# Optimization experiments

Measured on AMD Instinct MI355X. Metric: run time of the kernel, lower is better.

Reference implementation:

```python
import jax, jax.numpy as jnp
import numpy as np

B, S, D, H = 4, 2048, 2048, 16
Dh = D // H
BASE = 10000.0


def _rope_tables(seq_len, head_dim, dtype=jnp.float32):
    inv_freq = 1.0 / (BASE ** (jnp.arange(0, head_dim, 2, dtype=jnp.float32) / head_dim))
    t = jnp.arange(seq_len, dtype=jnp.float32)
    freqs = jnp.outer(t, inv_freq)              # [S, Dh/2]
    emb = jnp.concatenate([freqs, freqs], -1)   # [S, Dh]
    return jnp.cos(emb).astype(dtype), jnp.sin(emb).astype(dtype)


def _rotate_half(x):
    d = x.shape[-1] // 2
    return jnp.concatenate([-x[..., d:], x[..., :d]], axis=-1)


def setup_inputs() -> dict:
    key = jax.random.key(0)
    ks = jax.random.split(key, 5)
    std = D ** -0.5
    x = jax.random.normal(ks[0], (B, S, D), jnp.float32)
    Wq = jax.random.normal(ks[1], (D, D), jnp.float32) * std
    Wk = jax.random.normal(ks[2], (D, D), jnp.float32) * std
    Wv = jax.random.normal(ks[3], (D, D), jnp.float32) * std
    Wo = jax.random.normal(ks[4], (D, D), jnp.float32) * std
    attn_mask = jnp.triu(jnp.ones((S, S), dtype=bool), k=1)  # True = masked (causal)
    return {"x": x, "attn_mask": attn_mask, "Wq": Wq, "Wk": Wk, "Wv": Wv, "Wo": Wo}


def reference(x, attn_mask, Wq, Wk, Wv, Wo):
    b, s, d = x.shape
    # projections (nn.Linear: x @ W.T), split heads -> [B, H, S, Dh]
    q = (x @ Wq.T).reshape(b, s, H, Dh).transpose(0, 2, 1, 3)
    k = (x @ Wk.T).reshape(b, s, H, Dh).transpose(0, 2, 1, 3)
    v = (x @ Wv.T).reshape(b, s, H, Dh).transpose(0, 2, 1, 3)
    cos, sin = _rope_tables(s, Dh, x.dtype)     # [S, Dh]
    q = q * cos + _rotate_half(q) * sin
    k = k * cos + _rotate_half(k) * sin
    scale = Dh ** -0.5
    scores = jnp.einsum('bhqd,bhkd->bhqk', q, k) * scale
    scores = jnp.where(attn_mask[None, None, :, :], -jnp.inf, scores)
    weights = jax.nn.softmax(scores, axis=-1)
    out = jnp.einsum('bhqk,bhkd->bhqd', weights, v)
    out = out.transpose(0, 2, 1, 3).reshape(b, s, d)
    return out @ Wo.T
```

## Files before the change

kernel.cpp:

```cpp
#include <hip/hip_runtime.h>
#include <cstdint>
#include <cmath>

#define NB 4
#define NS 2048
#define ND 2048
#define NH 16
#define NDH 128
#define NM (NB*NS)

typedef unsigned short u16;
typedef __bf16 bf16x8 __attribute__((ext_vector_type(8)));
typedef u16    u16x8  __attribute__((ext_vector_type(8)));
typedef u16    u16x4  __attribute__((ext_vector_type(4)));
typedef float  f32x4  __attribute__((ext_vector_type(4)));
typedef float  f32x16 __attribute__((ext_vector_type(16)));
typedef unsigned u32x4_t __attribute__((ext_vector_type(4)));

__device__ __forceinline__ u16 f2bf(float f) {
  unsigned u = __float_as_uint(f);
  u += 0x7fffu + ((u >> 16) & 1u);
  return (u16)(u >> 16);
}
__device__ __forceinline__ float bf2f(u16 h) {
  return __uint_as_float(((unsigned)h) << 16);
}
__device__ __forceinline__ void gld16(const void* g, void* l) {
  __builtin_amdgcn_global_load_lds((__attribute__((address_space(1))) void*)g,
                                   (__attribute__((address_space(3))) void*)l,
                                   16, 0, 0);
}
__device__ __forceinline__ f32x4 mfma_bf16(bf16x8 a, bf16x8 b, f32x4 c) {
  return __builtin_amdgcn_mfma_f32_16x16x32_bf16(a, b, c, 0, 0, 0);
}
__device__ __forceinline__ f32x16 mfma32_bf16(bf16x8 a, bf16x8 b, f32x16 c) {
  return __builtin_amdgcn_mfma_f32_32x32x16_bf16(a, b, c, 0, 0, 0);
}
__device__ __forceinline__ unsigned cvtpk(float lo, float hi) {
  unsigned r;
  asm("v_cvt_pk_bf16_f32 %0, %1, %2" : "=v"(r) : "v"(lo), "v"(hi));
  return r;
}
__device__ __forceinline__ void p32swap(unsigned &a, unsigned &b) {
  asm volatile("v_permlane32_swap_b32 %0, %1" : "+v"(a), "+v"(b));
}

__global__ void cvt_bf16_kernel(const float* __restrict__ in, u16* __restrict__ out, int n8) {
  int i = blockIdx.x * 256 + threadIdx.x;
  if (i >= n8) return;
  const float4* p = (const float4*)in + (size_t)i * 2;
  float4 a = p[0], b = p[1];
  u16x8 r;
  r[0]=f2bf(a.x); r[1]=f2bf(a.y); r[2]=f2bf(a.z); r[3]=f2bf(a.w);
  r[4]=f2bf(b.x); r[5]=f2bf(b.y); r[6]=f2bf(b.z); r[7]=f2bf(b.w);
  ((u16x8*)out)[i] = r;
}

__global__ void rope_tables_kernel(float* __restrict__ cosT, float* __restrict__ sinT) {
  int s = blockIdx.x, d = threadIdx.x;
  double inv = pow(10000.0, -(double)d / 64.0);
  float ang = (float)((double)s * inv);
  cosT[s*64 + d] = cosf(ang);
  sinT[s*64 + d] = sinf(ang);
}

__global__ void rope_apply_kernel(u16* __restrict__ X, const float* __restrict__ cosT,
                                  const float* __restrict__ sinT) {
  int idx = blockIdx.x * 256 + threadIdx.x;
  int pc = idx & 7, h = (idx >> 3) & (NH - 1), m = idx >> 7;
  int s = m & (NS - 1);
  int d0 = pc * 8;
  size_t base = (size_t)m * ND + h * NDH + d0;
  u16x8 v0 = *(const u16x8*)(X + base);
  u16x8 v1 = *(const u16x8*)(X + base + 64);
  u16x8 r0, r1;
#pragma unroll
  for (int j = 0; j < 8; ++j) {
    float c  = cosT[s*64 + d0 + j];
    float sn = sinT[s*64 + d0 + j];
    float x0 = bf2f(v0[j]), x1 = bf2f(v1[j]);
    r0[j] = f2bf(x0 * c - x1 * sn);
    r1[j] = f2bf(x1 * c + x0 * sn);
  }
  *(u16x8*)(X + base)      = r0;
  *(u16x8*)(X + base + 64) = r1;
}

#define G_PHASE(BUF, KS, MH, LOADB, WAITV, STAGE) do {                            \
  bf16x8 af[4];                                                                   \
  _Pragma("unroll")                                                               \
  for (int mf = 0; mf < 4; ++mf)                                                  \
    af[mf] = *(const bf16x8*)(Asb + (BUF)*32768 + (KS)*16384 + arow + ((MH)*4+mf)*1024); \
  if (LOADB) {                                                                    \
    _Pragma("unroll")                                                             \
    for (int nf = 0; nf < 4; ++nf)                                                \
      bfr[nf] = *(const bf16x8*)(Bsb + (BUF)*32768 + (KS)*16384 + brow + nf*1024); \
  }                                                                               \
  STAGE;                                                                          \
  __builtin_amdgcn_s_setprio(1);                                                  \
  _Pragma("unroll")                                                               \
  for (int mf = 0; mf < 4; ++mf)                                                  \
    _Pragma("unroll")                                                             \
    for (int nf = 0; nf < 4; ++nf)                                                \
      acc[(MH)*4+mf][nf] = mfma_bf16(af[mf], bfr[nf], acc[(MH)*4+mf][nf]);        \
  __builtin_amdgcn_s_setprio(0);                                                  \
  if (WAITV) {                                                                    \
    asm volatile("s_waitcnt vmcnt(4)" ::: "memory");                              \
    __builtin_amdgcn_sched_barrier(0);                                            \
  }                                                                               \
  __builtin_amdgcn_s_barrier();                                                   \
  __builtin_amdgcn_sched_barrier(0);                                              \
} while (0)

template <typename OutT>
__global__ __launch_bounds__(512, 1) void gemm256_kernel(
    const u16* __restrict__ A, const u16* __restrict__ Bw, OutT* __restrict__ C,
    int Nd, int Kd) {
  __shared__ __align__(16) char Asb[65536];
  __shared__ __align__(16) char Bsb[65536];
  int tid = threadIdx.x;
  int wave = tid >> 6, lane = tid & 63;
  int li = lane & 15, lg = lane >> 4;
  int wr = wave >> 2, wc = wave & 3;
  int NTn = Nd >> 8;
  int cpx = (int)gridDim.x >> 3;
  int bid = (int)blockIdx.x;
  int swz = (bid & 7) * cpx + (bid >> 3);
  int m0 = (swz / NTn) << 8, n0 = (swz % NTn) << 8;

  int rswz = (lg * 16) ^ ((li & 3) << 4);
  int arow = (wr * 128 + li) * 64 + rswz;
  int brow = (wc *  64 + li) * 64 + rswz;

  int srow = wave * 16 + (lane >> 2);
  int scswz = ((lane & 3) * 16) ^ ((srow & 3) << 4);
  size_t rowB = (size_t)Kd * 2;
  const char* Asrc = (const char*)A + (size_t)(m0 + srow) * rowB + scswz;
  const char* Bsrc = (const char*)Bw + (size_t)(n0 + srow) * rowB + scswz;
  char* Adst = Asb + wave * 1024;
  char* Bdst = Bsb + wave * 1024;
  size_t half2 = rowB << 7;

  auto stageA = [&](int buf, int ks, int tile) {
    const char* s = Asrc + (size_t)tile * 128 + ks * 64;
    char* d = Adst + buf * 32768 + ks * 16384;
    gld16(s, d);
    gld16(s + half2, d + 8192);
  };
  auto stageB = [&](int buf, int ks, int tile) {
    const char* s = Bsrc + (size_t)tile * 128 + ks * 64;
    char* d = Bdst + buf * 32768 + ks * 16384;
    gld16(s, d);
    gld16(s + half2, d + 8192);
  };

  f32x4 acc[8][4] = {};
  bf16x8 bfr[4];

  int NKT = Kd >> 6;
  int NIT = NKT >> 1;

  stageA(0, 0, 0); stageA(0, 1, 0); stageB(0, 0, 0); stageB(0, 1, 0);
  stageA(1, 0, 1); stageB(1, 0, 1);
  asm volatile("s_waitcnt vmcnt(4)" ::: "memory");
  __builtin_amdgcn_sched_barrier(0);
  __builtin_amdgcn_s_barrier();
  __builtin_amdgcn_sched_barrier(0);

  for (int j = 0; j < NIT; ++j) {
    int t1  = 2*j + 1;
    int tn0 = (2*j + 2) & (NKT - 1);
    int tn1 = (2*j + 3) & (NKT - 1);
    G_PHASE(0, 0, 0, true,  false, { stageA(1, 1, t1);  });
    G_PHASE(0, 0, 1, false, false, { stageB(1, 1, t1);  });
    G_PHASE(0, 1, 1, true,  false, { stageA(0, 0, tn0); });
    G_PHASE(0, 1, 0, false, true,  { stageB(0, 0, tn0); });
    G_PHASE(1, 0, 0, true,  false, { stageA(0, 1, tn0); });
    G_PHASE(1, 0, 1, false, false, { stageB(0, 1, tn0); });
    G_PHASE(1, 1, 1, true,  false, { stageA(1, 0, tn1); });
    G_PHASE(1, 1, 0, false, true,  { stageB(1, 0, tn1); });
  }
  asm volatile("s_waitcnt vmcnt(0)" ::: "memory");

  int rbase = m0 + wr*128 + lg*4;
  int cbase = n0 + wc*64 + li;
#pragma unroll
  for (int am = 0; am < 8; ++am)
#pragma unroll
    for (int nf = 0; nf < 4; ++nf)
#pragma unroll
      for (int r = 0; r < 4; ++r) {
        size_t off = (size_t)(rbase + am*16 + r) * Nd + (cbase + nf*16);
        if constexpr (sizeof(OutT) == 2) C[off] = f2bf(acc[am][nf][r]);
        else                             C[off] = acc[am][nf][r];
      }
}

__global__ __launch_bounds__(512, 2) void flash_attn_kernel(
    const u16* __restrict__ Q, const u16* __restrict__ K, const u16* __restrict__ V,
    u16* __restrict__ O) {
  __shared__ __align__(16) u16 Ks[2*64*128];
  __shared__ __align__(16) u16 Vt[2*128*64];
  int tid = threadIdx.x, wv = tid >> 6, lane = tid & 63;
  int ql = lane & 31, hi = lane >> 5;
  int b = blockIdx.x >> 4, h = blockIdx.x & 15;
  int qt = (int)gridDim.y - 1 - (int)blockIdx.y;
  int q0 = qt << 8;
  int qw = q0 + wv*32;
  int qa = qw + ql;
  int swzl = (ql & 7) << 4;
  const float qscale = 0.08838834764831845f * 1.4426950408889634f;

  bf16x8 qf[8];
  {
    const u16* qp = Q + (size_t)(b*NS + qa) * ND + h*NDH + hi*8;
#pragma unroll
    for (int ds = 0; ds < 8; ++ds) {
      u16x8 t = *(const u16x8*)(qp + ds*16);
      u16x8 r;
#pragma unroll
      for (int j = 0; j < 8; ++j) r[j] = f2bf(bf2f(t[j]) * qscale);
      qf[ds] = *(bf16x8*)&r;
    }
  }
  f32x16 o0 = {}, o1 = {}, o2 = {}, o3 = {};
  float m_run = -INFINITY, l_run = 0.f;

  const char* Kg = (const char*)(K + (size_t)b*NS*ND + h*NDH);
  const char* Vg = (const char*)(V + (size_t)b*NS*ND + h*NDH);
  const int ROWB = ND * 2;

  int p   = tid & 31;
  int kvg = tid >> 5;

  auto issueKV = [&](int kv0, int buf, unsigned (&dlo)[4], unsigned (&dhi)[4]) {
    const char* vrow = Vg + (size_t)(kv0 + kvg*4) * ROWB;
#pragma unroll
    for (int j = 0; j < 4; ++j) {
      dlo[j] = *(const unsigned*)(vrow + j*ROWB + p*4);
      dhi[j] = *(const unsigned*)(vrow + j*ROWB + 128 + p*4);
    }
    char* ksb = (char*)Ks + buf*16384;
#pragma unroll
    for (int c = 0; c < 2; ++c) {
      int s = c*8192 + wv*1024 + lane*16;
      int row = s >> 8;
      int within = (s & 255) ^ ((row & 7) << 4);
      gld16(Kg + (size_t)(kv0 + row)*ROWB + within, ksb + c*8192 + wv*1024);
    }
    __builtin_amdgcn_sched_barrier(0);
  };

  auto dostep = [&](int kv0, int buf, const unsigned (&dlo)[4], const unsigned (&dhi)[4],
                    bool hasNext) {
    if (hasNext) asm volatile("s_waitcnt vmcnt(10)" ::: "memory");
    else         asm volatile("s_waitcnt vmcnt(0)"  ::: "memory");
    __builtin_amdgcn_sched_barrier(0);
    __builtin_amdgcn_s_barrier();
    __builtin_amdgcn_sched_barrier(0);

    char* vtb = (char*)Vt + buf*16384;
    const char* ksb = (const char*)Ks + buf*16384;

    {
      u16x4 rA, rB, rC, rD;
#pragma unroll
      for (int j = 0; j < 4; ++j) {
        rA[j] = (u16)dlo[j]; rB[j] = (u16)(dlo[j] >> 16);
        rC[j] = (u16)dhi[j]; rD[j] = (u16)(dhi[j] >> 16);
      }
      int a0 = ((2*p   )*128 + kvg*8) ^ (((2*p  ) & 7) << 4);
      int a1 = ((2*p+ 1)*128 + kvg*8) ^ (((2*p+1) & 7) << 4);
      int a2 = ((2*p+64)*128 + kvg*8) ^ (((2*p  ) & 7) << 4);
      int a3 = ((2*p+65)*128 + kvg*8) ^ (((2*p+1) & 7) << 4);
      *(u16x4*)(vtb + a0) = rA;
      *(u16x4*)(vtb + a1) = rB;
      *(u16x4*)(vtb + a2) = rC;
      *(u16x4*)(vtb + a3) = rD;
    }

    f32x16 p0 = {}, p1 = {};
    __builtin_amdgcn_s_setprio(1);
#pragma unroll
    for (int ds = 0; ds < 8; ++ds) {
      bf16x8 kf0 = *(const bf16x8*)(ksb + ((ql*256 + ds*32 + hi*16) ^ swzl));
      p0 = mfma32_bf16(kf0, qf[ds], p0);
      bf16x8 kf1 = *(const bf16x8*)(ksb + (((32+ql)*256 + ds*32 + hi*16) ^ swzl));
      p1 = mfma32_bf16(kf1, qf[ds], p1);
    }
    __builtin_amdgcn_s_setprio(0);

    if (kv0 + 63 > qw) {
      int thresh = qa - kv0 - 4*hi;
#pragma unroll
      for (int r = 0; r < 16; ++r) {
        int c0 = (r & 3) + 8*(r >> 2);
        p0[r] = (c0      > thresh) ? -INFINITY : p0[r];
        p1[r] = (c0 + 32 > thresh) ? -INFINITY : p1[r];
      }
    }

    float mx[16];
#pragma unroll
    for (int r = 0; r < 16; ++r) mx[r] = fmaxf(p0[r], p1[r]);
#pragma unroll
    for (int s = 8; s > 0; s >>= 1)
#pragma unroll
      for (int r = 0; r < 8; ++r) if (r < s) mx[r] = fmaxf(mx[r], mx[r + s]);
    float pmax = fmaxf(mx[0], __shfl_xor(mx[0], 32, 64));

    if (!__all(pmax <= m_run + 8.f)) {
      float mn = fmaxf(m_run, pmax);
      float corr = __builtin_amdgcn_exp2f(m_run - mn);
      m_run = mn; l_run *= corr;
#pragma unroll
      for (int r = 0; r < 16; ++r) {
        float cw = __shfl(corr, (r & 3) + 8*(r >> 2) + 4*hi, 64);
        o0[r] *= cw; o1[r] *= cw; o2[r] *= cw; o3[r] *= cw;
      }
    }

    float sm[16];
#pragma unroll
    for (int r = 0; r < 16; ++r) {
      p0[r] = __builtin_amdgcn_exp2f(p0[r] - m_run);
      p1[r] = __builtin_amdgcn_exp2f(p1[r] - m_run);
      sm[r] = p0[r] + p1[r];
    }
#pragma unroll
    for (int s = 8; s > 0; s >>= 1)
#pragma unroll
      for (int r = 0; r < 8; ++r) if (r < s) sm[r] += sm[r + s];
    l_run += sm[0] + __shfl_xor(sm[0], 32, 64);

    bf16x8 pa0, pa1, pa2, pa3;
#define MKPA(P, B, OUT) {                              \
      unsigned a0 = cvtpk(P[(B)+0], P[(B)+1]);         \
      unsigned b0 = cvtpk(P[(B)+4], P[(B)+5]);         \
      p32swap(a0, b0);                                 \
      unsigned a1 = cvtpk(P[(B)+2], P[(B)+3]);         \
      unsigned b1 = cvtpk(P[(B)+6], P[(B)+7]);         \
      p32swap(a1, b1);                                 \
      u32x4_t w; w[0]=a0; w[1]=a1; w[2]=b0; w[3]=b1;   \
      OUT = *(bf16x8*)&w; }
    MKPA(p0, 0, pa0)
    MKPA(p0, 8, pa1)
    MKPA(p1, 0, pa2)
    MKPA(p1, 8, pa3)
#undef MKPA

    asm volatile("s_waitcnt lgkmcnt(0)" ::: "memory");
    __builtin_amdgcn_sched_barrier(0);
    __builtin_amdgcn_s_barrier();
    __builtin_amdgcn_sched_barrier(0);

    __builtin_amdgcn_s_setprio(1);
#define PVT(OT, T) {                                                        \
      _Pragma("unroll")                                                     \
      for (int ks = 0; ks < 4; ++ks) {                                      \
        int a = ((((T)*32 + ql)*128 + ks*32 + hi*16) ^ swzl);               \
        bf16x8 vf = *(const bf16x8*)(vtb + a);                              \
        OT = mfma32_bf16(ks==0?pa0:ks==1?pa1:ks==2?pa2:pa3, vf, OT);        \
      } }
    PVT(o0, 0)
    PVT(o1, 1)
    PVT(o2, 2)
    PVT(o3, 3)
#undef PVT
    __builtin_amdgcn_s_setprio(0);
  };

  int nt = 4*qt + 4;
  unsigned dloA[4], dhiA[4], dloB[4], dhiB[4];
  issueKV(0, 0, dloA, dhiA);
  for (int t = 0; ; t += 2) {
    bool h1 = (t+1 < nt);
    if (h1) issueKV((t+1)*64, 1, dloB, dhiB);
    dostep(t*64, 0, dloA, dhiA, h1);
    if (!h1) break;
    bool h2 = (t+2 < nt);
    if (h2) issueKV((t+2)*64, 0, dloA, dhiA);
    dostep((t+1)*64, 1, dloB, dhiB, h2);
    if (!h2) break;
  }

  float inv = 1.0f / l_run;
#pragma unroll
  for (int r = 0; r < 16; ++r) {
    int crow = (r & 3) + 8*(r >> 2) + 4*hi;
    float iv = __shfl(inv, crow, 64);
    size_t base = (size_t)(b*NS + qw + crow) * ND + h*NDH + ql;
    O[base +  0] = f2bf(o0[r] * iv);
    O[base + 32] = f2bf(o1[r] * iv);
    O[base + 64] = f2bf(o2[r] * iv);
    O[base + 96] = f2bf(o3[r] * iv);
  }
}

extern "C" void kernel_launch(void* const* d_in, const int* in_sizes, int n_in,
                              void* d_out, int out_size, void* d_ws, size_t ws_size,
                              hipStream_t stream) {
  const float* x  = (const float*)d_in[0];
  const float* Wq = (const float*)d_in[2];
  const float* Wk = (const float*)d_in[3];
  const float* Wv = (const float*)d_in[4];
  const float* Wo = (const float*)d_in[5];

  char* ws = (char*)d_ws;
  const size_t SZ_MD = (size_t)NM * ND * 2;
  const size_t SZ_W  = (size_t)ND * ND * 2;
  u16* xb  = (u16*)(ws);
  u16* Qb  = (u16*)(ws + SZ_MD);
  u16* Kb  = (u16*)(ws + 2*SZ_MD);
  u16* Vb  = (u16*)(ws + 3*SZ_MD);
  u16* Ab  = (u16*)(ws + 4*SZ_MD);
  u16* Wqb = (u16*)(ws + 5*SZ_MD);
  u16* Wkb = (u16*)(ws + 5*SZ_MD + SZ_W);
  u16* Wvb = (u16*)(ws + 5*SZ_MD + 2*SZ_W);
  u16* Wob = (u16*)(ws + 5*SZ_MD + 3*SZ_W);
  float* cosT = (float*)(ws + 5*SZ_MD + 4*SZ_W);
  float* sinT = (float*)(ws + 5*SZ_MD + 4*SZ_W + (size_t)NS*64*4);
  size_t needed = 5*SZ_MD + 4*SZ_W + 2*(size_t)NS*64*4;
  if (ws_size < needed) return;

  {
    int n8 = (NM * ND) / 8;
    cvt_bf16_kernel<<<(n8 + 255)/256, 256, 0, stream>>>(x, xb, n8);
    int w8 = (ND * ND) / 8;
    cvt_bf16_kernel<<<(w8 + 255)/256, 256, 0, stream>>>(Wq, Wqb, w8);
    cvt_bf16_kernel<<<(w8 + 255)/256, 256, 0, stream>>>(Wk, Wkb, w8);
    cvt_bf16_kernel<<<(w8 + 255)/256, 256, 0, stream>>>(Wv, Wvb, w8);
    cvt_bf16_kernel<<<(w8 + 255)/256, 256, 0, stream>>>(Wo, Wob, w8);
  }
  rope_tables_kernel<<<NS, 64, 0, stream>>>(cosT, sinT);

  const int GEMM_GRID = (NM/256) * (ND/256);
  gemm256_kernel<u16><<<GEMM_GRID, 512, 0, stream>>>(xb, Wqb, Qb, ND, ND);
  gemm256_kernel<u16><<<GEMM_GRID, 512, 0, stream>>>(xb, Wkb, Kb, ND, ND);
  gemm256_kernel<u16><<<GEMM_GRID, 512, 0, stream>>>(xb, Wvb, Vb, ND, ND);

  {
    int nthr = NM * NH * 8;
    rope_apply_kernel<<<nthr/256, 256, 0, stream>>>(Qb, cosT, sinT);
    rope_apply_kernel<<<nthr/256, 256, 0, stream>>>(Kb, cosT, sinT);
  }

  flash_attn_kernel<<<dim3(NB*NH, NS/256), 512, 0, stream>>>(Qb, Kb, Vb, Ab);

  gemm256_kernel<float><<<GEMM_GRID, 512, 0, stream>>>(Ab, Wob, (float*)d_out, ND, ND);
}
```

Baseline: 433.4 us.

## Double-buffer GEMM LDS fragments in registers and request two blocks per CU

```diff
diff --git a/kernel.cpp b/kernel.cpp
--- a/kernel.cpp
+++ b/kernel.cpp
@@ -86,34 +86,28 @@
   *(u16x8*)(X + base + 64) = r1;
 }
 
-#define G_PHASE(BUF, KS, MH, LOADB, WAITV, STAGE) do {                            \
-  bf16x8 af[4];                                                                   \
+#define RD_A(SET, BUF, KS, MH)                                                    \
   _Pragma("unroll")                                                               \
   for (int mf = 0; mf < 4; ++mf)                                                  \
-    af[mf] = *(const bf16x8*)(Asb + (BUF)*32768 + (KS)*16384 + arow + ((MH)*4+mf)*1024); \
-  if (LOADB) {                                                                    \
-    _Pragma("unroll")                                                             \
-    for (int nf = 0; nf < 4; ++nf)                                                \
-      bfr[nf] = *(const bf16x8*)(Bsb + (BUF)*32768 + (KS)*16384 + brow + nf*1024); \
-  }                                                                               \
-  STAGE;                                                                          \
+    SET[mf] = *(const bf16x8*)(Asb + (BUF)*32768 + (KS)*16384 + arow + ((MH)*4+mf)*1024);
+#define RD_B(SET, BUF, KS)                                                        \
+  _Pragma("unroll")                                                               \
+  for (int nf = 0; nf < 4; ++nf)                                                  \
+    SET[nf] = *(const bf16x8*)(Bsb + (BUF)*32768 + (KS)*16384 + brow + nf*1024);
+#define MM(ASET, BSET, MH)                                                        \
   __builtin_amdgcn_s_setprio(1);                                                  \
   _Pragma("unroll")                                                               \
   for (int mf = 0; mf < 4; ++mf)                                                  \
     _Pragma("unroll")                                                             \
     for (int nf = 0; nf < 4; ++nf)                                                \
-      acc[(MH)*4+mf][nf] = mfma_bf16(af[mf], bfr[nf], acc[(MH)*4+mf][nf]);        \
-  __builtin_amdgcn_s_setprio(0);                                                  \
-  if (WAITV) {                                                                    \
-    asm volatile("s_waitcnt vmcnt(4)" ::: "memory");                              \
-    __builtin_amdgcn_sched_barrier(0);                                            \
-  }                                                                               \
-  __builtin_amdgcn_s_barrier();                                                   \
-  __builtin_amdgcn_sched_barrier(0);                                              \
-} while (0)
+      acc[(MH)*4+mf][nf] = mfma_bf16(ASET[mf], BSET[nf], acc[(MH)*4+mf][nf]);     \
+  __builtin_amdgcn_s_setprio(0);
+#define BARX do { __builtin_amdgcn_s_barrier(); __builtin_amdgcn_sched_barrier(0); } while (0)
+#define VM4  do { asm volatile("s_waitcnt vmcnt(4)" ::: "memory"); \
+                  __builtin_amdgcn_sched_barrier(0); } while (0)
 
 template <typename OutT>
-__global__ __launch_bounds__(512, 1) void gemm256_kernel(
+__global__ __launch_bounds__(512, 2) void gemm256_kernel(
     const u16* __restrict__ A, const u16* __restrict__ Bw, OutT* __restrict__ C,
     int Nd, int Kd) {
   __shared__ __align__(16) char Asb[65536];
@@ -155,7 +149,7 @@
   };
 
   f32x4 acc[8][4] = {};
-  bf16x8 bfr[4];
+  bf16x8 af_x[4], af_y[4], bf_x[4], bf_y[4];
 
   int NKT = Kd >> 6;
   int NIT = NKT >> 1;
@@ -171,14 +165,38 @@
     int t1  = 2*j + 1;
     int tn0 = (2*j + 2) & (NKT - 1);
     int tn1 = (2*j + 3) & (NKT - 1);
-    G_PHASE(0, 0, 0, true,  false, { stageA(1, 1, t1);  });
-    G_PHASE(0, 0, 1, false, false, { stageB(1, 1, t1);  });
-    G_PHASE(0, 1, 1, true,  false, { stageA(0, 0, tn0); });
-    G_PHASE(0, 1, 0, false, true,  { stageB(0, 0, tn0); });
-    G_PHASE(1, 0, 0, true,  false, { stageA(0, 1, tn0); });
-    G_PHASE(1, 0, 1, false, false, { stageB(0, 1, tn0); });
-    G_PHASE(1, 1, 1, true,  false, { stageA(1, 0, tn1); });
-    G_PHASE(1, 1, 0, false, true,  { stageB(1, 0, tn1); });
+    RD_A(af_x, 0, 0, 0) RD_B(bf_x, 0, 0)
+    stageA(1, 1, t1);
+    RD_A(af_y, 0, 0, 1)
+    MM(af_x, bf_x, 0)
+    BARX;
+    stageB(1, 1, t1);
+    RD_A(af_x, 0, 1, 1) RD_B(bf_y, 0, 1)
+    MM(af_y, bf_x, 1)
+    BARX;
+    stageA(0, 0, tn0);
+    RD_A(af_y, 0, 1, 0)
+    MM(af_x, bf_y, 1)
+    BARX;
+    stageB(0, 0, tn0);
+    MM(af_y, bf_y, 0)
+    VM4; BARX;
+    RD_A(af_x, 1, 0, 0) RD_B(bf_x, 1, 0)
+    stageA(0, 1, tn0);
+    RD_A(af_y, 1, 0, 1)
+    MM(af_x, bf_x, 0)
+    BARX;
+    stageB(0, 1, tn0);
+    RD_A(af_x, 1, 1, 1) RD_B(bf_y, 1, 1)
+    MM(af_y, bf_x, 1)
+    BARX;
+    stageA(1, 0, tn1);
+    RD_A(af_y, 1, 1, 0)
+    MM(af_x, bf_y, 1)
+    BARX;
+    stageB(1, 0, tn1);
+    MM(af_y, bf_y, 0)
+    VM4; BARX;
   }
   asm volatile("s_waitcnt vmcnt(0)" ::: "memory");
 
```

Result: no change. 437.2 us (+0.9%).
